# Kernel tuning notes

Hardware: AMD Instinct MI355X
Metric: run time of the kernel (lower is better)

## Reference

```python
import jax, jax.numpy as jnp
import numpy as np

V, EMB, HID, ENC = 32000, 512, 1024, 1024
B, T, TB = 64, 512, 512
PAD = 0


def setup_inputs() -> dict:
    key = jax.random.key(0)
    kk = jax.random.split(key, 24)
    w = lambda k, s: jax.random.normal(k, s, dtype=jnp.float32) * 0.02
    a = lambda k, s: jax.random.normal(k, s, dtype=jnp.float32)
    emb_table = w(kk[0], (V, EMB)).at[PAD].set(0.0)  # padding_idx row zeroed
    IN = EMB + ENC + HID  # lstm input size
    return {
        "y": jax.random.randint(kk[1], (B,), 0, V),
        "h": a(kk[2], (B, HID)),
        "c": a(kk[3], (B, HID)),
        "enc_out": a(kk[4], (B, T, ENC)),
        "bwd_states": a(kk[5], (B, TB, HID)),
        "src_ids": jax.random.randint(kk[6], (B, T), 0, V),
        "src_mask": jnp.ones((B, T), dtype=jnp.int32),
        "emb_table": emb_table,
        "W_ih": w(kk[7], (4 * HID, IN)),
        "W_hh": w(kk[8], (4 * HID, HID)),
        "b_ih": jnp.zeros((4 * HID,), jnp.float32),
        "b_hh": jnp.zeros((4 * HID,), jnp.float32),
        "Wq_e": w(kk[9], (HID, HID)),
        "Wk_e": w(kk[10], (HID, ENC)),
        "v_e": w(kk[11], (HID,)),
        "Wq_b": w(kk[12], (HID, HID)),
        "Wk_b": w(kk[13], (HID, HID)),
        "v_b": w(kk[14], (HID,)),
        "Wp": w(kk[15], (V, HID)),
        "bp": jnp.zeros((V,), jnp.float32),
        "wc": w(kk[16], (ENC,)),
        "ws": w(kk[17], (HID,)),
        "wy": w(kk[18], (EMB,)),
        "pg_b": jnp.zeros((), jnp.float32),
    }


def _bahdanau(query, keys, Wq, Wk, v, mask=None):
    # query [B,H], keys [B,T,D] -> context [B,D], attn [B,T]
    q = query @ Wq.T                                  # [B,A]
    k = jnp.einsum("btd,ad->bta", keys, Wk)           # [B,T,A]
    e = jnp.einsum("bta,a->bt", jnp.tanh(q[:, None, :] + k), v)
    if mask is not None:
        e = jnp.where(mask == 0, jnp.finfo(e.dtype).min, e)
    attn = jax.nn.softmax(e, axis=-1)
    ctx = jnp.einsum("bt,btd->bd", attn, keys)
    return ctx, attn


def reference(y, h, c, enc_out, bwd_states, src_ids, src_mask, emb_table,
              W_ih, W_hh, b_ih, b_hh, Wq_e, Wk_e, v_e, Wq_b, Wk_b, v_b,
              Wp, bp, wc, ws, wy, pg_b):
    emb = emb_table[y]                                # [B,EMB]
    query = h                                         # state[0].squeeze(0)
    c_enc, attn_enc = _bahdanau(query, enc_out, Wq_e, Wk_e, v_e, src_mask)
    c_bwd, _ = _bahdanau(query, bwd_states, Wq_b, Wk_b, v_b)
    x = jnp.concatenate([emb, c_enc, c_bwd], axis=-1)  # [B,EMB+ENC+HID]
    gates = x @ W_ih.T + h @ W_hh.T + b_ih + b_hh      # [B,4H], torch order i,f,g,o
    i, f, g, o = jnp.split(gates, 4, axis=-1)
    c_new = jax.nn.sigmoid(f) * c + jax.nn.sigmoid(i) * jnp.tanh(g)
    h_new = jax.nn.sigmoid(o) * jnp.tanh(c_new)
    vocab_dist = jax.nn.softmax(h_new @ Wp.T + bp, axis=-1)  # [B,V]
    p_gen = jax.nn.sigmoid(c_enc @ wc + h_new @ ws + emb @ wy + pg_b)[:, None]
    p_vocab = p_gen * vocab_dist
    copy_mask = (src_ids < V).astype(vocab_dist.dtype)
    safe_ids = jnp.minimum(src_ids, V - 1)
    contrib = (1.0 - p_gen) * attn_enc * copy_mask     # [B,T]
    scatter = jax.vmap(lambda idx, val: jnp.zeros((V,), val.dtype).at[idx].add(val))(safe_ids, contrib)
    final_dist = p_vocab + scatter
    return final_dist, h_new, c_new
```

## Files before the change

kernel.cpp:

```cpp
#include <hip/hip_runtime.h>
#include <hip/hip_bf16.h>

#define VSZ   32000
#define EMBD  512
#define HIDD  1024
#define BB    64
#define TSEQ  512
#define G4    4096

typedef short bf16x8 __attribute__((ext_vector_type(8)));
typedef float f32x4  __attribute__((ext_vector_type(4)));
typedef float f32x16 __attribute__((ext_vector_type(16)));

__device__ __forceinline__ float sigmoid_f(float x){ return 1.0f/(1.0f+__expf(-x)); }
__device__ __forceinline__ float fast_tanh(float x){
  float e = __expf(2.0f*x);
  return 1.0f - 2.0f*__builtin_amdgcn_rcpf(e + 1.0f);
}
__device__ __forceinline__ short f2bfs(float x){
  unsigned u = __float_as_uint(x);
  unsigned r = (u + 0x7FFFu + ((u>>16)&1u)) >> 16;
  return (short)r;
}
__device__ __forceinline__ bf16x8 cvt8(float4 a, float4 b){
  bf16x8 p;
  p[0]=f2bfs(a.x); p[1]=f2bfs(a.y); p[2]=f2bfs(a.z); p[3]=f2bfs(a.w);
  p[4]=f2bfs(b.x); p[5]=f2bfs(b.y); p[6]=f2bfs(b.z); p[7]=f2bfs(b.w);
  return p;
}
__device__ __forceinline__ float wave_sum(float x){
  #pragma unroll
  for (int off=32; off>0; off>>=1) x += __shfl_xor(x, off);
  return x;
}
__device__ __forceinline__ float wave_max(float x){
  #pragma unroll
  for (int off=32; off>0; off>>=1) x = fmaxf(x, __shfl_xor(x, off));
  return x;
}

__global__ __launch_bounds__(256) void k_pack(const float* __restrict__ Wk,
                                              short* __restrict__ dst){
  int id = blockIdx.x*256 + threadIdx.x;
  int l = id & 63, s = (id>>6) & 63, nt = id >> 12;
  const float* src = Wk + (size_t)(nt*32 + (l&31))*1024 + s*16 + (l>>5)*8;
  float4 f0 = ((const float4*)src)[0], f1 = ((const float4*)src)[1];
  *(bf16x8*)(dst + (size_t)id*8) = cvt8(f0, f1);
}

__global__ __launch_bounds__(256) void k_prep_h(const float* __restrict__ h,
                                                short* __restrict__ xb){
  int id = blockIdx.x*256 + threadIdx.x;
  int b = id >> 7, d = (id & 127)*8;
  const float4* s = (const float4*)(h + (size_t)b*HIDD + d);
  *(bf16x8*)(xb + (size_t)b*3584 + 2560 + d) = cvt8(s[0], s[1]);
}

__global__ __launch_bounds__(256) void k_prep_x2(const float* __restrict__ tab,
                                                 const int* __restrict__ y,
                                                 const float* __restrict__ ctxe,
                                                 const float* __restrict__ ctxb,
                                                 short* __restrict__ xb){
  int id = blockIdx.x*256 + threadIdx.x;
  if (id >= 64*320) return;
  int b = id / 320, off = (id % 320)*8;
  const float* src;
  if (off < 512)        src = tab  + (size_t)y[b]*EMBD + off;
  else if (off < 1536)  src = ctxe + (size_t)b*HIDD + (off-512);
  else                  src = ctxb + (size_t)b*HIDD + (off-1536);
  float4 f0 = ((const float4*)src)[0], f1 = ((const float4*)src)[1];
  *(bf16x8*)(xb + (size_t)b*3584 + off) = cvt8(f0, f1);
}

__global__ __launch_bounds__(256) void k_mm64(
    const short* __restrict__ A0, int lda0, const float* __restrict__ B0, int ldb0, int K0, float* __restrict__ out0, int ldo0,
    const short* __restrict__ A1, int lda1, const float* __restrict__ B1, int ldb1, int K1, float* __restrict__ out1, int ldo1){
  const short* A; const float* B; float* out; int lda, ldb, K, ldo;
  if (blockIdx.z == 0){ A=A0; B=B0; out=out0; lda=lda0; ldb=ldb0; K=K0; ldo=ldo0; }
  else                { A=A1; B=B1; out=out1; lda=lda1; ldb=ldb1; K=K1; ldo=ldo1; }
  int tid = threadIdx.x, l = tid & 63, w = tid >> 6;
  int l15 = l & 15, l4 = l >> 4;
  int n0 = blockIdx.x*256 + w*64;
  int kper = K / gridDim.y;
  int dbeg = blockIdx.y * kper, dend = dbeg + kper;
  f32x4 acc[4][4];
  #pragma unroll
  for (int i=0;i<4;i++)
    #pragma unroll
    for (int j=0;j<4;j++)
      #pragma unroll
      for (int r=0;r<4;r++) acc[i][j][r]=0.f;
  for (int d0=dbeg; d0<dend; d0+=32){
    bf16x8 af[4];
    #pragma unroll
    for (int ms=0; ms<4; ms++)
      af[ms] = *(const bf16x8*)(A + (size_t)(ms*16 + l15)*lda + d0 + l4*8);
    bf16x8 bfr[4];
    #pragma unroll
    for (int ni=0; ni<4; ni++){
      const float* bp = B + (size_t)(n0 + ni*16 + l15)*ldb + d0 + l4*8;
      float4 f0 = ((const float4*)bp)[0], f1 = ((const float4*)bp)[1];
      bfr[ni] = cvt8(f0, f1);
    }
    #pragma unroll
    for (int ms=0; ms<4; ms++)
      #pragma unroll
      for (int ni=0; ni<4; ni++)
        acc[ms][ni] = __builtin_amdgcn_mfma_f32_16x16x32_bf16(af[ms], bfr[ni], acc[ms][ni], 0,0,0);
  }
  float* op = out + (size_t)blockIdx.y * 64 * ldo;
  #pragma unroll
  for (int ms=0; ms<4; ms++)
    #pragma unroll
    for (int ni=0; ni<4; ni++)
      #pragma unroll
      for (int r=0; r<4; r++){
        int m = ms*16 + l4*4 + r;
        op[(size_t)m*ldo + n0 + ni*16 + l15] = acc[ms][ni][r];
      }
}

__global__ __launch_bounds__(256,2) void k_energy(
    const float* __restrict__ enc, const float* __restrict__ bwd,
    const short* __restrict__ pke, const short* __restrict__ pkb,
    const float* __restrict__ qpe, const float* __restrict__ qpb,
    const float* __restrict__ ve, const float* __restrict__ vb,
    float* __restrict__ ep_out){
  __shared__ short A_s[2][64*128];
  __shared__ float ebuf[4][64];
  int bx = blockIdx.x;
  int half = bx & 1, att = (bx>>1) & 1, t0 = (bx>>2)*64;
  const float* keys = att ? bwd : enc;
  const short* pk   = att ? pkb : pke;
  const float* qp   = att ? qpb : qpe;
  const float* v    = att ? vb  : ve;
  int b = blockIdx.y;
  int tid = threadIdx.x, l = tid & 63, w = tid >> 6;
  int lhi = l >> 5, l31 = l & 31;

  int sr = tid >> 2, sf = tid & 3;
  const float4* ssrc = (const float4*)(keys + ((size_t)(b*TSEQ + t0 + sr))*1024) + sf*8;
  char* swb = (char*)A_s + sr*256;
  int wsw[4];
  #pragma unroll
  for (int j=0;j<4;j++) wsw[j] = (((sf*4+j)<<4) ^ ((sr&15)<<4));

  const bf16x8* Bp = ((const bf16x8*)pk) + ((size_t)(half*16 + w*4)*64)*64 + l;
  int rb0 = l31*256, rb1 = (l31+32)*256;
  int xorv = (l31&15)<<4;

  f32x16 acc0[4], acc1[4];
  #pragma unroll
  for (int at=0; at<4; at++)
    #pragma unroll
    for (int r=0;r<16;r++){ acc0[at][r]=0.f; acc1[at][r]=0.f; }

  float4 st[8];
  #pragma unroll
  for (int i=0;i<8;i++) st[i] = ssrc[i];
  #pragma unroll
  for (int j=0;j<4;j++) *(bf16x8*)(swb + wsw[j]) = cvt8(st[2*j], st[2*j+1]);
  __syncthreads();
  #pragma unroll
  for (int i=0;i<8;i++) st[i] = ssrc[32 + i];

  for (int c=0; c<8; ++c){
    const char* base = (const char*)A_s + (c&1)*16384;
    #pragma unroll
    for (int ss=0; ss<8; ++ss){
      int s = c*8 + ss;
      bf16x8 b0 = Bp[(0*64+s)*64];
      bf16x8 b1 = Bp[(1*64+s)*64];
      bf16x8 b2 = Bp[(2*64+s)*64];
      bf16x8 b3 = Bp[(3*64+s)*64];
      int off = (((ss*2 + lhi)<<4) ^ xorv);
      bf16x8 a0 = *(const bf16x8*)(base + rb0 + off);
      bf16x8 a1 = *(const bf16x8*)(base + rb1 + off);
      acc0[0] = __builtin_amdgcn_mfma_f32_32x32x16_bf16(a0, b0, acc0[0], 0,0,0);
      acc1[0] = __builtin_amdgcn_mfma_f32_32x32x16_bf16(a1, b0, acc1[0], 0,0,0);
      acc0[1] = __builtin_amdgcn_mfma_f32_32x32x16_bf16(a0, b1, acc0[1], 0,0,0);
      acc1[1] = __builtin_amdgcn_mfma_f32_32x32x16_bf16(a1, b1, acc1[1], 0,0,0);
      acc0[2] = __builtin_amdgcn_mfma_f32_32x32x16_bf16(a0, b2, acc0[2], 0,0,0);
      acc1[2] = __builtin_amdgcn_mfma_f32_32x32x16_bf16(a1, b2, acc1[2], 0,0,0);
      acc0[3] = __builtin_amdgcn_mfma_f32_32x32x16_bf16(a0, b3, acc0[3], 0,0,0);
      acc1[3] = __builtin_amdgcn_mfma_f32_32x32x16_bf16(a1, b3, acc1[3], 0,0,0);
    }
    if (c < 7){
      char* dst = (char*)A_s + ((c+1)&1)*16384 + sr*256;
      #pragma unroll
      for (int j=0;j<4;j++) *(bf16x8*)(dst + wsw[j]) = cvt8(st[2*j], st[2*j+1]);
      if (c < 6){
        #pragma unroll
        for (int i=0;i<8;i++) st[i] = ssrc[(c+2)*32 + i];
      }
    }
    __syncthreads();
  }

  float ep0[16], ep1[16];
  #pragma unroll
  for (int r=0;r<16;r++){ ep0[r]=0.f; ep1[r]=0.f; }
  #pragma unroll
  for (int at=0; at<4; at++){
    int a = half*512 + w*128 + at*32 + l31;
    float qv = qp[(size_t)b*HIDD + a] + qp[65536 + (size_t)b*HIDD + a];
    float vv = v[a];
    #pragma unroll
    for (int r=0;r<16;r++){
      ep0[r] += vv * fast_tanh(qv + acc0[at][r]);
      ep1[r] += vv * fast_tanh(qv + acc1[at][r]);
    }
  }
  #pragma unroll
  for (int r=0;r<16;r++){
    float x = ep0[r];
    x += __shfl_xor(x,1); x += __shfl_xor(x,2); x += __shfl_xor(x,4);
    x += __shfl_xor(x,8); x += __shfl_xor(x,16);
    ep0[r] = x;
    float y = ep1[r];
    y += __shfl_xor(y,1); y += __shfl_xor(y,2); y += __shfl_xor(y,4);
    y += __shfl_xor(y,8); y += __shfl_xor(y,16);
    ep1[r] = y;
  }
  if (l31 == 0){
    #pragma unroll
    for (int r=0;r<16;r++){
      int t = (r&3) + 8*(r>>2) + 4*lhi;
      ebuf[w][t]      = ep0[r];
      ebuf[w][t + 32] = ep1[r];
    }
  }
  __syncthreads();
  if (tid < 64){
    float s = 0.f;
    #pragma unroll
    for (int ww=0; ww<4; ww++) s += ebuf[ww][tid];
    ep_out[(((size_t)att*2 + half)*BB + b)*TSEQ + t0 + tid] = s;
  }
}

__global__ __launch_bounds__(256) void k_softmax_t(const float* __restrict__ ep,
                                                   const int* __restrict__ mask,
                                                   float* __restrict__ att_e,
                                                   float* __restrict__ att_b){
  int b = blockIdx.x, att = blockIdx.y;
  const float* p0 = ep + (((size_t)att*2 + 0)*BB + b)*TSEQ;
  const float* p1 = ep + (((size_t)att*2 + 1)*BB + b)*TSEQ;
  float* e = (att ? att_b : att_e) + (size_t)b*TSEQ;
  __shared__ float red[8];
  int tid = threadIdx.x, lane = tid & 63, w = tid >> 6;
  float v0 = p0[tid] + p1[tid];
  float v1 = p0[tid+256] + p1[tid+256];
  if (att==0){
    if (mask[(size_t)b*TSEQ + tid]==0)      v0 = -3.4e38f;
    if (mask[(size_t)b*TSEQ + tid+256]==0)  v1 = -3.4e38f;
  }
  float m = wave_max(fmaxf(v0, v1));
  if (lane==0) red[w] = m;
  __syncthreads();
  m = fmaxf(fmaxf(red[0],red[1]), fmaxf(red[2],red[3]));
  float x0 = __expf(v0-m), x1 = __expf(v1-m);
  float s = wave_sum(x0+x1);
  if (lane==0) red[4+w] = s;
  __syncthreads();
  s = red[4]+red[5]+red[6]+red[7];
  float inv = 1.0f/s;
  e[tid] = x0*inv; e[tid+256] = x1*inv;
}

__global__ __launch_bounds__(256) void k_ctx(const float* __restrict__ enc,
                                             const float* __restrict__ bwdst,
                                             const float* __restrict__ att_e,
                                             const float* __restrict__ att_b,
                                             float* __restrict__ ctxp){
  int b = blockIdx.x, sel = blockIdx.y, s = blockIdx.z;
  const float* keys = (sel ? bwdst : enc) + ((size_t)b*TSEQ + s*64)*1024;
  const float* att  = (sel ? att_b : att_e) + (size_t)b*TSEQ + s*64;
  int tid = threadIdx.x;
  float acc[4] = {0.f,0.f,0.f,0.f};
  for (int t=0;t<64;t++){
    float a = att[t];
    #pragma unroll
    for (int i=0;i<4;i++) acc[i] += a*keys[(size_t)t*1024 + i*256 + tid];
  }
  float* o = ctxp + (((size_t)sel*BB + b)*8 + s)*1024;
  #pragma unroll
  for (int i=0;i<4;i++) o[i*256+tid] = acc[i];
}

__global__ __launch_bounds__(256) void k_ctxred(const float* __restrict__ ctxp,
                                                float* __restrict__ ctx_e,
                                                float* __restrict__ ctx_b){
  int id = blockIdx.x*256 + threadIdx.x;
  int sel = id >> 16; int rem = id & 65535; int b = rem >> 10; int d = rem & 1023;
  const float* p = ctxp + (((size_t)sel*BB + b)*8)*1024 + d;
  float s = 0.f;
  #pragma unroll
  for (int i=0;i<8;i++) s += p[i*1024];
  (sel ? ctx_b : ctx_e)[(size_t)b*HIDD + d] = s;
}

__global__ __launch_bounds__(256) void k_lstm(const float* __restrict__ gp,
                                              const float* __restrict__ b_ih,
                                              const float* __restrict__ b_hh,
                                              const float* __restrict__ c_old,
                                              float* __restrict__ out,
                                              short* __restrict__ hb){
  int id = blockIdx.x*256 + threadIdx.x;
  int b = id >> 10, j = id & 1023;
  size_t base = (size_t)b*G4;
  float gs[4];
  #pragma unroll
  for (int g=0; g<4; g++){
    int col = g*1024 + j;
    float s = b_ih[col] + b_hh[col];
    #pragma unroll
    for (int k=0;k<8;k++) s += gp[(size_t)k*(64*G4) + base + col];
    gs[g] = s;
  }
  float ig = sigmoid_f(gs[0]);
  float fg = sigmoid_f(gs[1]);
  float gg = tanhf(gs[2]);
  float og = sigmoid_f(gs[3]);
  float cn = fg*c_old[id] + ig*gg;
  float hn = og*tanhf(cn);
  out[(size_t)BB*VSZ + id] = hn;
  out[(size_t)BB*VSZ + (size_t)BB*HIDD + id] = cn;
  hb[id] = f2bfs(hn);
}

__global__ __launch_bounds__(256) void k_vocab2(const short* __restrict__ hb,
                                                const float* __restrict__ Wp,
                                                const float* __restrict__ bp,
                                                float* __restrict__ out){
  int tid = threadIdx.x, l = tid & 63, w = tid >> 6;
  int l15 = l & 15, l4 = l >> 4;
  int mh = w >> 1;
  int n0 = blockIdx.x*128 + (w&1)*64;
  f32x4 acc[2][4];
  #pragma unroll
  for (int i=0;i<2;i++)
    #pragma unroll
    for (int j=0;j<4;j++)
      #pragma unroll
      for (int r=0;r<4;r++) acc[i][j][r]=0.f;
  for (int d0=0; d0<1024; d0+=32){
    bf16x8 af[2];
    #pragma unroll
    for (int ms=0; ms<2; ms++)
      af[ms] = *(const bf16x8*)(hb + (size_t)(mh*32 + ms*16 + l15)*1024 + d0 + l4*8);
    bf16x8 bfr[4];
    #pragma unroll
    for (int ni=0; ni<4; ni++){
      const float* bpp = Wp + (size_t)(n0 + ni*16 + l15)*1024 + d0 + l4*8;
      float4 f0 = ((const float4*)bpp)[0], f1 = ((const float4*)bpp)[1];
      bfr[ni] = cvt8(f0, f1);
    }
    #pragma unroll
    for (int ms=0; ms<2; ms++)
      #pragma unroll
      for (int ni=0; ni<4; ni++)
        acc[ms][ni] = __builtin_amdgcn_mfma_f32_16x16x32_bf16(af[ms], bfr[ni], acc[ms][ni], 0,0,0);
  }
  #pragma unroll
  for (int ms=0; ms<2; ms++)
    #pragma unroll
    for (int ni=0; ni<4; ni++)
      #pragma unroll
      for (int r=0; r<4; r++){
        int m = mh*32 + ms*16 + l4*4 + r;
        int n = n0 + ni*16 + l15;
        out[(size_t)m*VSZ + n] = acc[ms][ni][r] + bp[n];
      }
}

__global__ __launch_bounds__(1024) void k_final(const float* __restrict__ ctxe,
                                                const float* __restrict__ tab,
                                                const int* __restrict__ y,
                                                const float* __restrict__ wc,
                                                const float* __restrict__ wsv,
                                                const float* __restrict__ wy,
                                                const float* __restrict__ pgb,
                                                float* __restrict__ out,
                                                float* __restrict__ pgen_ws){
  __shared__ float red[32];
  int b = blockIdx.x, tid = threadIdx.x, lane = tid & 63, w = tid >> 6;
  const float* hn = out + (size_t)BB*VSZ + (size_t)b*HIDD;
  float acc = ctxe[(size_t)b*HIDD + tid]*wc[tid] + hn[tid]*wsv[tid];
  if (tid < 512) acc += tab[(size_t)y[b]*EMBD + tid]*wy[tid];
  acc = wave_sum(acc);
  if (lane==0) red[w] = acc;
  __syncthreads();
  float s0 = pgb[0];
  #pragma unroll
  for (int i=0;i<16;i++) s0 += red[i];
  float pg = sigmoid_f(s0);
  if (tid==0) pgen_ws[b] = pg;
  __syncthreads();

  float* row = out + (size_t)b*VSZ;
  float m = -3.4e38f;
  for (int i=tid;i<VSZ;i+=1024) m = fmaxf(m, row[i]);
  m = wave_max(m);
  if (lane==0) red[w] = m;
  __syncthreads();
  #pragma unroll
  for (int i=0;i<16;i++) m = fmaxf(m, red[i]);
  float s = 0.f;
  for (int i=tid;i<VSZ;i+=1024) s += __expf(row[i]-m);
  s = wave_sum(s);
  if (lane==0) red[16+w] = s;
  __syncthreads();
  float tot = 0.f;
  #pragma unroll
  for (int i=0;i<16;i++) tot += red[16+i];
  float scale = pg / tot;
  for (int i=tid;i<VSZ;i+=1024) row[i] = __expf(row[i]-m)*scale;
}

__global__ __launch_bounds__(256) void k_scatter(const int* __restrict__ src_ids,
                                                 const float* __restrict__ att_e,
                                                 const float* __restrict__ pgen_ws,
                                                 float* __restrict__ out){
  int id = blockIdx.x*256 + threadIdx.x;
  int b = id >> 9;
  float pg = pgen_ws[b];
  int sid = src_ids[id];
  float contrib = (1.0f - pg) * att_e[id] * (sid < VSZ ? 1.0f : 0.0f);
  int safe = sid < VSZ-1 ? sid : VSZ-1;
  atomicAdd(&out[(size_t)b*VSZ + safe], contrib);
}

extern "C" void kernel_launch(void* const* d_in, const int* in_sizes, int n_in,
                              void* d_out, int out_size, void* d_ws, size_t ws_size,
                              hipStream_t stream){
  const int*   y     = (const int*)d_in[0];
  const float* h     = (const float*)d_in[1];
  const float* c     = (const float*)d_in[2];
  const float* enc   = (const float*)d_in[3];
  const float* bwd   = (const float*)d_in[4];
  const int*   sids  = (const int*)d_in[5];
  const int*   smask = (const int*)d_in[6];
  const float* tab   = (const float*)d_in[7];
  const float* W_ih  = (const float*)d_in[8];
  const float* W_hh  = (const float*)d_in[9];
  const float* b_ih  = (const float*)d_in[10];
  const float* b_hh  = (const float*)d_in[11];
  const float* Wq_e  = (const float*)d_in[12];
  const float* Wk_e  = (const float*)d_in[13];
  const float* v_e   = (const float*)d_in[14];
  const float* Wq_b  = (const float*)d_in[15];
  const float* Wk_b  = (const float*)d_in[16];
  const float* v_b   = (const float*)d_in[17];
  const float* Wp    = (const float*)d_in[18];
  const float* bp    = (const float*)d_in[19];
  const float* wc    = (const float*)d_in[20];
  const float* wsv   = (const float*)d_in[21];
  const float* wy    = (const float*)d_in[22];
  const float* pgb   = (const float*)d_in[23];
  float* out = (float*)d_out;

  float* W = (float*)d_ws;
  float* ws_qpe  = W; W += 2*BB*HIDD;
  float* ws_qpb  = W; W += 2*BB*HIDD;
  float* ws_ep   = W; W += 4*BB*TSEQ;
  float* ws_atte = W; W += BB*TSEQ;
  float* ws_attb = W; W += BB*TSEQ;
  float* ws_ctxe = W; W += BB*HIDD;
  float* ws_ctxb = W; W += BB*HIDD;
  float* ws_ctxp = W; W += 2*BB*8*1024;
  float* ws_pgen = W; W += 64;
  float* ws_gp   = W; W += 8*BB*G4;
  short* xb      = (short*)W; W += (BB*3584)/2;
  short* hb      = (short*)W; W += (BB*HIDD)/2;
  short* pk_e    = (short*)W; W += (HIDD*HIDD)/2;
  short* pk_b    = (short*)W; W += (HIDD*HIDD)/2;

  k_pack<<<512, 256, 0, stream>>>(Wk_e, pk_e);
  k_pack<<<512, 256, 0, stream>>>(Wk_b, pk_b);
  k_prep_h<<<32, 256, 0, stream>>>(h, xb);
  k_mm64<<<dim3(4,2,2), 256, 0, stream>>>(
      xb+2560, 3584, Wq_e, 1024, 1024, ws_qpe, 1024,
      xb+2560, 3584, Wq_b, 1024, 1024, ws_qpb, 1024);
  k_energy<<<dim3(32,BB), 256, 0, stream>>>(enc, bwd, pk_e, pk_b,
      ws_qpe, ws_qpb, v_e, v_b, ws_ep);
  k_softmax_t<<<dim3(BB,2), 256, 0, stream>>>(ws_ep, smask, ws_atte, ws_attb);
  k_ctx<<<dim3(BB,2,8), 256, 0, stream>>>(enc, bwd, ws_atte, ws_attb, ws_ctxp);
  k_ctxred<<<512, 256, 0, stream>>>(ws_ctxp, ws_ctxe, ws_ctxb);
  k_prep_x2<<<80, 256, 0, stream>>>(tab, y, ws_ctxe, ws_ctxb, xb);
  k_mm64<<<dim3(16,4,2), 256, 0, stream>>>(
      xb,      3584, W_ih, 2560, 2560, ws_gp,             G4,
      xb+2560, 3584, W_hh, 1024, 1024, ws_gp + 4*BB*G4,   G4);
  k_lstm<<<256, 256, 0, stream>>>(ws_gp, b_ih, b_hh, c, out, hb);
  k_vocab2<<<250, 256, 0, stream>>>(hb, Wp, bp, out);
  k_final<<<BB, 1024, 0, stream>>>(ws_ctxe, tab, y, wc, wsv, wy, pgb, out, ws_pgen);
  k_scatter<<<128, 256, 0, stream>>>(sids, ws_atte, ws_pgen, out);
}
```

Baseline: 432.9 us.

## Retile attention energy GEMM to 128x128 tiles with LDS-staged weights and XCD mapping

Restructures the energy kernel from 64-row tiles with B fragments read straight from global memory into 128(t)x128(a) tiles. Both the keys (converted to bf16) and the repacked, swizzled Wk blocks are staged in LDS, the latter via global_load_lds, and the MFMAs change to 16x16x32. Blocks are remapped across XCDs so neighbouring blocks share a batch row's keys in L2. The attention dimension is split into 8 partial energy outputs, so the softmax now sums 8 partials. This trades fewer redundant weight reads and better cache locality for re-reading the fp32 keys once per attention slice (8x) and single-buffered LDS with extra barriers.

```diff
diff --git a/kernel.cpp b/kernel.cpp
--- a/kernel.cpp
+++ b/kernel.cpp
@@ -10,7 +10,12 @@
 
 typedef short bf16x8 __attribute__((ext_vector_type(8)));
 typedef float f32x4  __attribute__((ext_vector_type(4)));
-typedef float f32x16 __attribute__((ext_vector_type(16)));
+
+typedef __attribute__((address_space(3))) unsigned       lds_u32_t;
+typedef __attribute__((address_space(1))) const unsigned glb_u32_t;
+__device__ __forceinline__ void gload16(const void* g, void* l){
+  __builtin_amdgcn_global_load_lds((glb_u32_t*)g, (lds_u32_t*)l, 16, 0, 0);
+}
 
 __device__ __forceinline__ float sigmoid_f(float x){ return 1.0f/(1.0f+__expf(-x)); }
 __device__ __forceinline__ float fast_tanh(float x){
@@ -42,8 +47,9 @@
 __global__ __launch_bounds__(256) void k_pack(const float* __restrict__ Wk,
                                               short* __restrict__ dst){
   int id = blockIdx.x*256 + threadIdx.x;
-  int l = id & 63, s = (id>>6) & 63, nt = id >> 12;
-  const float* src = Wk + (size_t)(nt*32 + (l&31))*1024 + s*16 + (l>>5)*8;
+  int a = id >> 7, g = id & 127;
+  int gs = (g & ~7) | ((g & 7) ^ (a & 7));
+  const float* src = Wk + (size_t)a*1024 + gs*8;
   float4 f0 = ((const float4*)src)[0], f1 = ((const float4*)src)[1];
   *(bf16x8*)(dst + (size_t)id*8) = cvt8(f0, f1);
 }
@@ -126,117 +132,120 @@
     const float* __restrict__ qpe, const float* __restrict__ qpb,
     const float* __restrict__ ve, const float* __restrict__ vb,
     float* __restrict__ ep_out){
-  __shared__ short A_s[2][64*128];
-  __shared__ float ebuf[4][64];
-  int bx = blockIdx.x;
-  int half = bx & 1, att = (bx>>1) & 1, t0 = (bx>>2)*64;
+  __shared__ short A_s[128*64];
+  __shared__ short B_s[128*64];
+  __shared__ float ebuf[2][128];
+
+  int wg = blockIdx.x;
+  int xcd = wg & 7, idx = wg >> 3;
+  int tglob = xcd*64 + (idx >> 3);
+  int A0 = idx & 7;
+  int att = tglob >> 8;
+  int tt  = tglob & 255;
+  int b = tt >> 2, t0 = (tt & 3)*128;
+
   const float* keys = att ? bwd : enc;
   const short* pk   = att ? pkb : pke;
   const float* qp   = att ? qpb : qpe;
   const float* v    = att ? vb  : ve;
-  int b = blockIdx.y;
+
   int tid = threadIdx.x, l = tid & 63, w = tid >> 6;
-  int lhi = l >> 5, l31 = l & 31;
-
-  int sr = tid >> 2, sf = tid & 3;
-  const float4* ssrc = (const float4*)(keys + ((size_t)(b*TSEQ + t0 + sr))*1024) + sf*8;
-  char* swb = (char*)A_s + sr*256;
-  int wsw[4];
-  #pragma unroll
-  for (int j=0;j<4;j++) wsw[j] = (((sf*4+j)<<4) ^ ((sr&15)<<4));
-
-  const bf16x8* Bp = ((const bf16x8*)pk) + ((size_t)(half*16 + w*4)*64)*64 + l;
-  int rb0 = l31*256, rb1 = (l31+32)*256;
-  int xorv = (l31&15)<<4;
-
-  f32x16 acc0[4], acc1[4];
-  #pragma unroll
-  for (int at=0; at<4; at++)
-    #pragma unroll
-    for (int r=0;r<16;r++){ acc0[at][r]=0.f; acc1[at][r]=0.f; }
+  int l15 = l & 15, l4 = l >> 4;
+  int wr = w >> 1, wc = w & 1;
+
+  int sr = tid >> 1, hf = tid & 1;
+  const float4* asrc4 = (const float4*)(keys + ((size_t)b*TSEQ + t0 + sr)*1024 + hf*32);
+  char* awr = (char*)A_s + sr*128;
+  int sw = (sr & 7) << 4;
+  int aw0 = (hf*64 +  0) ^ sw;
+  int aw1 = (hf*64 + 16) ^ sw;
+  int aw2 = (hf*64 + 32) ^ sw;
+  int aw3 = (hf*64 + 48) ^ sw;
+
+  const char* bsrc = (const char*)pk + ((size_t)(A0*128 + w*32 + (l>>3)))*2048 + (l&7)*16;
+
+  f32x4 acc[4][4];
+  #pragma unroll
+  for (int i=0;i<4;i++)
+    #pragma unroll
+    for (int j=0;j<4;j++)
+      #pragma unroll
+      for (int r=0;r<4;r++) acc[i][j][r]=0.f;
 
   float4 st[8];
   #pragma unroll
-  for (int i=0;i<8;i++) st[i] = ssrc[i];
-  #pragma unroll
-  for (int j=0;j<4;j++) *(bf16x8*)(swb + wsw[j]) = cvt8(st[2*j], st[2*j+1]);
-  __syncthreads();
-  #pragma unroll
-  for (int i=0;i<8;i++) st[i] = ssrc[32 + i];
-
-  for (int c=0; c<8; ++c){
-    const char* base = (const char*)A_s + (c&1)*16384;
-    #pragma unroll
-    for (int ss=0; ss<8; ++ss){
-      int s = c*8 + ss;
-      bf16x8 b0 = Bp[(0*64+s)*64];
-      bf16x8 b1 = Bp[(1*64+s)*64];
-      bf16x8 b2 = Bp[(2*64+s)*64];
-      bf16x8 b3 = Bp[(3*64+s)*64];
-      int off = (((ss*2 + lhi)<<4) ^ xorv);
-      bf16x8 a0 = *(const bf16x8*)(base + rb0 + off);
-      bf16x8 a1 = *(const bf16x8*)(base + rb1 + off);
-      acc0[0] = __builtin_amdgcn_mfma_f32_32x32x16_bf16(a0, b0, acc0[0], 0,0,0);
-      acc1[0] = __builtin_amdgcn_mfma_f32_32x32x16_bf16(a1, b0, acc1[0], 0,0,0);
-      acc0[1] = __builtin_amdgcn_mfma_f32_32x32x16_bf16(a0, b1, acc0[1], 0,0,0);
-      acc1[1] = __builtin_amdgcn_mfma_f32_32x32x16_bf16(a1, b1, acc1[1], 0,0,0);
-      acc0[2] = __builtin_amdgcn_mfma_f32_32x32x16_bf16(a0, b2, acc0[2], 0,0,0);
-      acc1[2] = __builtin_amdgcn_mfma_f32_32x32x16_bf16(a1, b2, acc1[2], 0,0,0);
-      acc0[3] = __builtin_amdgcn_mfma_f32_32x32x16_bf16(a0, b3, acc0[3], 0,0,0);
-      acc1[3] = __builtin_amdgcn_mfma_f32_32x32x16_bf16(a1, b3, acc1[3], 0,0,0);
+  for (int i=0;i<8;i++) st[i] = asrc4[i];
+
+  for (int c=0; c<16; ++c){
+    if (c) __syncthreads();
+    *(bf16x8*)(awr + aw0) = cvt8(st[0], st[1]);
+    *(bf16x8*)(awr + aw1) = cvt8(st[2], st[3]);
+    *(bf16x8*)(awr + aw2) = cvt8(st[4], st[5]);
+    *(bf16x8*)(awr + aw3) = cvt8(st[6], st[7]);
+    #pragma unroll
+    for (int k=0;k<4;k++)
+      gload16(bsrc + (size_t)c*128 + (size_t)k*16384, (char*)B_s + w*4096 + k*1024);
+    __syncthreads();
+    if (c < 15){
+      #pragma unroll
+      for (int i=0;i<8;i++) st[i] = asrc4[(c+1)*16 + i];
     }
-    if (c < 7){
-      char* dst = (char*)A_s + ((c+1)&1)*16384 + sr*256;
-      #pragma unroll
-      for (int j=0;j<4;j++) *(bf16x8*)(dst + wsw[j]) = cvt8(st[2*j], st[2*j+1]);
-      if (c < 6){
+    #pragma unroll
+    for (int ks=0; ks<2; ks++){
+      bf16x8 af[4], bf[4];
+      #pragma unroll
+      for (int ms=0; ms<4; ms++){
+        int row = wr*64 + ms*16 + l15;
+        af[ms] = *(const bf16x8*)((char*)A_s + row*128 + ((ks*64 + l4*16) ^ ((row&7)<<4)));
+      }
+      #pragma unroll
+      for (int ni=0; ni<4; ni++){
+        int row = wc*64 + ni*16 + l15;
+        bf[ni] = *(const bf16x8*)((char*)B_s + row*128 + ((ks*64 + l4*16) ^ ((row&7)<<4)));
+      }
+      #pragma unroll
+      for (int ms=0; ms<4; ms++)
         #pragma unroll
-        for (int i=0;i<8;i++) st[i] = ssrc[(c+2)*32 + i];
-      }
+        for (int ni=0; ni<4; ni++)
+          acc[ms][ni] = __builtin_amdgcn_mfma_f32_16x16x32_bf16(af[ms], bf[ni], acc[ms][ni], 0,0,0);
     }
-    __syncthreads();
-  }
-
-  float ep0[16], ep1[16];
-  #pragma unroll
-  for (int r=0;r<16;r++){ ep0[r]=0.f; ep1[r]=0.f; }
-  #pragma unroll
-  for (int at=0; at<4; at++){
-    int a = half*512 + w*128 + at*32 + l31;
-    float qv = qp[(size_t)b*HIDD + a] + qp[65536 + (size_t)b*HIDD + a];
-    float vv = v[a];
-    #pragma unroll
-    for (int r=0;r<16;r++){
-      ep0[r] += vv * fast_tanh(qv + acc0[at][r]);
-      ep1[r] += vv * fast_tanh(qv + acc1[at][r]);
+  }
+
+  float qv[4], vv[4];
+  #pragma unroll
+  for (int ni=0; ni<4; ni++){
+    int a = A0*128 + wc*64 + ni*16 + l15;
+    qv[ni] = qp[(size_t)b*HIDD + a] + qp[65536 + (size_t)b*HIDD + a];
+    vv[ni] = v[a];
+  }
+  float es[16];
+  #pragma unroll
+  for (int ms=0; ms<4; ms++)
+    #pragma unroll
+    for (int r=0; r<4; r++){
+      float s = 0.f;
+      #pragma unroll
+      for (int ni=0; ni<4; ni++)
+        s += vv[ni]*fast_tanh(qv[ni] + acc[ms][ni][r]);
+      es[ms*4+r] = s;
     }
-  }
-  #pragma unroll
-  for (int r=0;r<16;r++){
-    float x = ep0[r];
-    x += __shfl_xor(x,1); x += __shfl_xor(x,2); x += __shfl_xor(x,4);
-    x += __shfl_xor(x,8); x += __shfl_xor(x,16);
-    ep0[r] = x;
-    float y = ep1[r];
-    y += __shfl_xor(y,1); y += __shfl_xor(y,2); y += __shfl_xor(y,4);
-    y += __shfl_xor(y,8); y += __shfl_xor(y,16);
-    ep1[r] = y;
-  }
-  if (l31 == 0){
-    #pragma unroll
-    for (int r=0;r<16;r++){
-      int t = (r&3) + 8*(r>>2) + 4*lhi;
-      ebuf[w][t]      = ep0[r];
-      ebuf[w][t + 32] = ep1[r];
-    }
-  }
-  __syncthreads();
-  if (tid < 64){
-    float s = 0.f;
-    #pragma unroll
-    for (int ww=0; ww<4; ww++) s += ebuf[ww][tid];
-    ep_out[(((size_t)att*2 + half)*BB + b)*TSEQ + t0 + tid] = s;
-  }
+  #pragma unroll
+  for (int i=0;i<16;i++){
+    float x = es[i];
+    x += __shfl_xor(x,1); x += __shfl_xor(x,2);
+    x += __shfl_xor(x,4); x += __shfl_xor(x,8);
+    es[i] = x;
+  }
+  if (l15 == 0){
+    #pragma unroll
+    for (int ms=0; ms<4; ms++)
+      #pragma unroll
+      for (int r=0; r<4; r++)
+        ebuf[wc][wr*64 + ms*16 + l4*4 + r] = es[ms*4+r];
+  }
+  __syncthreads();
+  if (tid < 128)
+    ep_out[(((size_t)att*8 + A0)*BB + b)*TSEQ + t0 + tid] = ebuf[0][tid] + ebuf[1][tid];
 }
 
 __global__ __launch_bounds__(256) void k_softmax_t(const float* __restrict__ ep,
@@ -244,13 +253,15 @@
                                                    float* __restrict__ att_e,
                                                    float* __restrict__ att_b){
   int b = blockIdx.x, att = blockIdx.y;
-  const float* p0 = ep + (((size_t)att*2 + 0)*BB + b)*TSEQ;
-  const float* p1 = ep + (((size_t)att*2 + 1)*BB + b)*TSEQ;
   float* e = (att ? att_b : att_e) + (size_t)b*TSEQ;
   __shared__ float red[8];
   int tid = threadIdx.x, lane = tid & 63, w = tid >> 6;
-  float v0 = p0[tid] + p1[tid];
-  float v1 = p0[tid+256] + p1[tid+256];
+  float v0 = 0.f, v1 = 0.f;
+  #pragma unroll
+  for (int i=0;i<8;i++){
+    const float* p = ep + (((size_t)att*8 + i)*BB + b)*TSEQ;
+    v0 += p[tid]; v1 += p[tid+256];
+  }
   if (att==0){
     if (mask[(size_t)b*TSEQ + tid]==0)      v0 = -3.4e38f;
     if (mask[(size_t)b*TSEQ + tid+256]==0)  v1 = -3.4e38f;
@@ -463,7 +474,7 @@
   float* W = (float*)d_ws;
   float* ws_qpe  = W; W += 2*BB*HIDD;
   float* ws_qpb  = W; W += 2*BB*HIDD;
-  float* ws_ep   = W; W += 4*BB*TSEQ;
+  float* ws_ep   = W; W += 2*8*BB*TSEQ;
   float* ws_atte = W; W += BB*TSEQ;
   float* ws_attb = W; W += BB*TSEQ;
   float* ws_ctxe = W; W += BB*HIDD;
@@ -482,7 +493,7 @@
   k_mm64<<<dim3(4,2,2), 256, 0, stream>>>(
       xb+2560, 3584, Wq_e, 1024, 1024, ws_qpe, 1024,
       xb+2560, 3584, Wq_b, 1024, 1024, ws_qpb, 1024);
-  k_energy<<<dim3(32,BB), 256, 0, stream>>>(enc, bwd, pk_e, pk_b,
+  k_energy<<<4096, 256, 0, stream>>>(enc, bwd, pk_e, pk_b,
       ws_qpe, ws_qpb, v_e, v_b, ws_ep);
   k_softmax_t<<<dim3(BB,2), 256, 0, stream>>>(ws_ep, smask, ws_atte, ws_attb);
   k_ctx<<<dim3(BB,2,8), 256, 0, stream>>>(enc, bwd, ws_atte, ws_attb, ws_ctxp);
```

Measured after the change: 495.6 us. 14.5% more time.
